# Kernel tuning notes

Hardware: AMD Instinct MI355X
Metric: run time of the kernel (lower is better)

The kernel has to match this reference:

```python
import jax, jax.numpy as jnp
import numpy as np

NUM_NODES = 100000
OUT_CHANNELS = 32
NUM_EDGES = 3200000


def setup_inputs() -> dict:
    key = jax.random.key(0)
    k1, k2, k3 = jax.random.split(key, 3)
    edge_index = jax.random.randint(k1, (2, NUM_EDGES), 0, NUM_NODES, dtype=jnp.int64)
    # nn.Linear init: weight [out, in], uniform(-1/sqrt(in), 1/sqrt(in))
    bound = 1.0 / np.sqrt(NUM_NODES)
    W = jax.random.uniform(k2, (OUT_CHANNELS, NUM_NODES), jnp.float32, -bound, bound)
    b = jax.random.uniform(k3, (OUT_CHANNELS,), jnp.float32, -bound, bound)
    return {"edge_index": edge_index, "W": W, "b": b}


def reference(edge_index, W, b):
    # LINK forward: A = sparse COO [N, num_nodes] with 1.0 per edge (duplicates sum),
    # logits = A @ W.T + b. Implemented as gather + segment_sum (no dense A).
    row = edge_index[0]
    col = edge_index[1]
    row = row - row.min()  # faithful to `row = row - row.min()`
    gathered = jnp.take(W.T, col, axis=0)  # [E, out_channels]
    logits = jax.ops.segment_sum(gathered, row, num_segments=NUM_NODES)  # [N, out]
    return logits + b
```

## Files before the change

kernel.cpp:

```cpp
#include <hip/hip_runtime.h>

#define NUM_NODES 100000
#define OUT_CH 32
#define NUM_EDGES 3200000

#define RPB 128
#define NB 782
#define NBG 783
#define CAP2 5120
#define FTPB 1024
#define TRB 782
#define BINB 250
#define TILE 12800
#define KPT 13
#define TPB 512

static __device__ __forceinline__ unsigned short f32_to_bf16_rne(float f) {
    unsigned u = __float_as_uint(f);
    unsigned r = u + 0x7FFFu + ((u >> 16) & 1u);
    return (unsigned short)(r >> 16);
}
static __device__ __forceinline__ float bf16_to_f32(unsigned short h) {
    return __uint_as_float(((unsigned)h) << 16);
}

__global__ void __launch_bounds__(FTPB)
fused_pre(const float* __restrict__ W, ushort4* __restrict__ Wt,
          const int* __restrict__ edge, int* __restrict__ partmin,
          int* __restrict__ bcount, unsigned int* __restrict__ bin) {
    int bk = blockIdx.x;
    int t  = threadIdx.x;
    if (bk < TRB) {
        __shared__ float tile[32][129];
        int tx = t & 127, ty = t >> 7;
        int colBase = bk * 128;
        int col = colBase + tx;
        if (col < NUM_NODES) {
            #pragma unroll
            for (int k = 0; k < 4; k++) {
                int c = ty + 8 * k;
                tile[c][tx] = W[(size_t)c * NUM_NODES + col];
            }
        }
        __syncthreads();
        int lc = t >> 3, q = t & 7;
        int ocol = colBase + lc;
        if (ocol < NUM_NODES) {
            ushort4 o;
            o.x = f32_to_bf16_rne(tile[q * 4 + 0][lc]);
            o.y = f32_to_bf16_rne(tile[q * 4 + 1][lc]);
            o.z = f32_to_bf16_rne(tile[q * 4 + 2][lc]);
            o.w = f32_to_bf16_rne(tile[q * 4 + 3][lc]);
            Wt[(size_t)ocol * 8 + q] = o;
        }
    } else {
        int mb = bk - TRB;
        __shared__ int cnt[NB];
        __shared__ int cur[NB];
        __shared__ int wm[16];
        for (int i = t; i < NB; i += FTPB) cnt[i] = 0;
        __syncthreads();
        int base = mb * TILE;
        unsigned int ent[KPT];
        int bb[KPT];
        int rm = 0x7fffffff;
        #pragma unroll
        for (int k = 0; k < KPT; k++) {
            int o = k * FTPB + t;
            bb[k] = -1;
            if (o < TILE) {
                int e = base + o;
                int r = edge[e];
                int c = edge[NUM_EDGES + e];
                rm = min(rm, r);
                int b = r >> 7;
                bb[k]  = b;
                ent[k] = ((unsigned int)(r & 127) << 17) | (unsigned int)c;
                atomicAdd(&cnt[b], 1);
            }
        }
        #pragma unroll
        for (int off = 32; off > 0; off >>= 1) rm = min(rm, __shfl_down(rm, off, 64));
        if ((t & 63) == 0) wm[t >> 6] = rm;
        __syncthreads();
        if (t == 0) {
            int m = wm[0];
            #pragma unroll
            for (int w = 1; w < 16; w++) m = min(m, wm[w]);
            partmin[mb] = m;
        }
        for (int i = t; i < NB; i += FTPB) cur[i] = cnt[i] ? atomicAdd(&bcount[i], cnt[i]) : 0;
        __syncthreads();
        #pragma unroll
        for (int k = 0; k < KPT; k++) {
            if (bb[k] >= 0) {
                int pos = atomicAdd(&cur[bb[k]], 1);
                if (pos < CAP2) bin[(size_t)bb[k] * CAP2 + pos] = ent[k];
            }
        }
    }
}

__global__ void __launch_bounds__(TPB)
bucket_gather(const unsigned int* __restrict__ bin, const int* __restrict__ bcount,
              const int* __restrict__ partmin,
              const ushort4* __restrict__ Wt, const float* __restrict__ b,
              float* __restrict__ out) {
    __shared__ int cnt2[RPB * 8];
    __shared__ int cur2[RPB * 8];
    __shared__ int rowstart[RPB];
    __shared__ int rowcnt[RPB];
    __shared__ int scn[RPB];
    __shared__ int lcol[CAP2];
    __shared__ int wmin[8];
    __shared__ int rminS;

    int t = threadIdx.x;
    int bk = blockIdx.x;
    int pm = (t < BINB) ? partmin[t] : 0x7fffffff;
    #pragma unroll
    for (int off = 32; off > 0; off >>= 1) pm = min(pm, __shfl_down(pm, off, 64));
    if ((t & 63) == 0) wmin[t >> 6] = pm;

    int n = (bk < NB) ? bcount[bk] : 0;
    if (n > CAP2) n = CAP2;
    const unsigned int* mybin = bin + (size_t)bk * CAP2;

    for (int i = t; i < RPB * 8; i += TPB) cnt2[i] = 0;
    __syncthreads();
    if (t == 0) {
        int m = wmin[0];
        #pragma unroll
        for (int w = 1; w < 8; w++) m = min(m, wmin[w]);
        rminS = m;
    }

    for (int i = t; i < n; i += TPB) {
        unsigned int p = mybin[i];
        int lr  = p >> 17;
        int seg = (p & 0x1FFFF) >> 14;
        atomicAdd(&cnt2[(lr << 3) | seg], 1);
    }
    __syncthreads();

    if (t < RPB) {
        int s = 0;
        #pragma unroll
        for (int k = 0; k < 8; k++) s += cnt2[(t << 3) | k];
        rowcnt[t] = s;
        scn[t] = s;
    }
    __syncthreads();
    for (int off = 1; off < RPB; off <<= 1) {
        int v = (t < RPB && t >= off) ? scn[t - off] : 0;
        __syncthreads();
        if (t < RPB) scn[t] += v;
        __syncthreads();
    }
    if (t < RPB) {
        int rs = scn[t] - rowcnt[t];
        rowstart[t] = rs;
        int run = rs;
        #pragma unroll
        for (int k = 0; k < 8; k++) { cur2[(t << 3) | k] = run; run += cnt2[(t << 3) | k]; }
    }
    __syncthreads();

    for (int i = t; i < n; i += TPB) {
        unsigned int p = mybin[i];
        int lr = p >> 17;
        int c  = p & 0x1FFFF;
        int pos = atomicAdd(&cur2[(lr << 3) | (c >> 14)], 1);
        lcol[pos] = c;
    }
    __syncthreads();

    int g   = t >> 3;
    int sub = t & 7;
    float4 bias = ((const float4*)b)[sub];
    int rmin = rminS;
    int lrA = g, lrB = g + 64;
    int outA = bk * RPB + lrA - rmin;
    int outB = bk * RPB + lrB - rmin;
    bool vA = (unsigned)outA < NUM_NODES;
    bool vB = (unsigned)outB < NUM_NODES;
    int iA = rowstart[lrA], eA = iA + rowcnt[lrA];
    int iB = rowstart[lrB], eB = iB + rowcnt[lrB];
    if (!vA) { iA = eA = 0; }
    if (!vB) { iB = eB = 0; }
    float4 accA = bias, accB = bias;
    int nPair = min(eA - iA, eB - iB);
    for (int k = 0; k < nPair; k++) {
        ushort4 wA = Wt[(size_t)lcol[iA + k] * 8 + sub];
        ushort4 wB = Wt[(size_t)lcol[iB + k] * 8 + sub];
        accA.x += bf16_to_f32(wA.x); accA.y += bf16_to_f32(wA.y);
        accA.z += bf16_to_f32(wA.z); accA.w += bf16_to_f32(wA.w);
        accB.x += bf16_to_f32(wB.x); accB.y += bf16_to_f32(wB.y);
        accB.z += bf16_to_f32(wB.z); accB.w += bf16_to_f32(wB.w);
    }
    iA += nPair; iB += nPair;
    for (; iA < eA; iA++) {
        ushort4 w = Wt[(size_t)lcol[iA] * 8 + sub];
        accA.x += bf16_to_f32(w.x); accA.y += bf16_to_f32(w.y);
        accA.z += bf16_to_f32(w.z); accA.w += bf16_to_f32(w.w);
    }
    for (; iB < eB; iB++) {
        ushort4 w = Wt[(size_t)lcol[iB] * 8 + sub];
        accB.x += bf16_to_f32(w.x); accB.y += bf16_to_f32(w.y);
        accB.z += bf16_to_f32(w.z); accB.w += bf16_to_f32(w.w);
    }
    if (vA) ((float4*)out)[(size_t)outA * 8 + sub] = accA;
    if (vB) ((float4*)out)[(size_t)outB * 8 + sub] = accB;
}

extern "C" void kernel_launch(void* const* d_in, const int* in_sizes, int n_in,
                              void* d_out, int out_size, void* d_ws, size_t ws_size,
                              hipStream_t stream) {
    const int*   edge = (const int*)d_in[0];
    const float* W    = (const float*)d_in[1];
    const float* b    = (const float*)d_in[2];
    float* out = (float*)d_out;

    char* ws = (char*)d_ws;
    int*          partmin = (int*)ws;
    int*          bcount  = (int*)(ws + 1024);
    ushort4*      Wt      = (ushort4*)(ws + 8192);
    unsigned int* bin     = (unsigned int*)(ws + 6422528);

    hipMemsetAsync(bcount, 0, NBG * sizeof(int), stream);
    fused_pre<<<TRB + BINB, FTPB, 0, stream>>>(W, Wt, edge, partmin, bcount, bin);
    bucket_gather<<<NBG, TPB, 0, stream>>>(bin, bcount, partmin, Wt, b, out);
}
```

Baseline: 151.9 us.

## Split each row bucket across two blocks and unroll the gather loop by four

The gather kernel now launches two 256-thread blocks per 128-row bucket. Each block filters the bucket's entries down to its own 64 rows, which shrinks shared memory and raises the block count to improve occupancy and latency hiding. The inner accumulation loop is unrolled by four, so eight independent Wt loads are in flight per iteration. The cost is that each bucket's bin is read twice. The per-half column buffer (CAPH) could overflow if a half-bucket holds more than 2560 entries.

```diff
diff --git a/kernel.cpp b/kernel.cpp
--- a/kernel.cpp
+++ b/kernel.cpp
@@ -13,7 +13,9 @@
 #define BINB 250
 #define TILE 12800
 #define KPT 13
-#define TPB 512
+#define GTPB 256
+#define CAPH 2560
+#define GGRID 1568
 
 static __device__ __forceinline__ unsigned short f32_to_bf16_rne(float f) {
     unsigned u = __float_as_uint(f);
@@ -89,7 +91,8 @@
             for (int w = 1; w < 16; w++) m = min(m, wm[w]);
             partmin[mb] = m;
         }
-        for (int i = t; i < NB; i += FTPB) cur[i] = cnt[i] ? atomicAdd(&bcount[i], cnt[i]) : 0;
+        for (int i = t; i < NB; i += FTPB)
+            cur[i] = cnt[i] ? atomicAdd(&bcount[i], cnt[i]) : 0;
         __syncthreads();
         #pragma unroll
         for (int k = 0; k < KPT; k++) {
@@ -101,49 +104,50 @@
     }
 }
 
-__global__ void __launch_bounds__(TPB)
+__global__ void __launch_bounds__(GTPB)
 bucket_gather(const unsigned int* __restrict__ bin, const int* __restrict__ bcount,
               const int* __restrict__ partmin,
               const ushort4* __restrict__ Wt, const float* __restrict__ b,
               float* __restrict__ out) {
-    __shared__ int cnt2[RPB * 8];
-    __shared__ int cur2[RPB * 8];
-    __shared__ int rowstart[RPB];
-    __shared__ int rowcnt[RPB];
-    __shared__ int scn[RPB];
-    __shared__ int lcol[CAP2];
-    __shared__ int wmin[8];
+    __shared__ int cnt2[64 * 8];
+    __shared__ int cur2[64 * 8];
+    __shared__ int rowstart[64];
+    __shared__ int rowcnt[64];
+    __shared__ int scn[64];
+    __shared__ int lcol[CAPH];
+    __shared__ int wmin[4];
     __shared__ int rminS;
 
-    int t = threadIdx.x;
+    int t  = threadIdx.x;
     int bk = blockIdx.x;
+    int gb   = ((bk >> 4) << 3) | (bk & 7);
+    int hbit = ((bk >> 3) & 1) << 6;
+
     int pm = (t < BINB) ? partmin[t] : 0x7fffffff;
     #pragma unroll
     for (int off = 32; off > 0; off >>= 1) pm = min(pm, __shfl_down(pm, off, 64));
     if ((t & 63) == 0) wmin[t >> 6] = pm;
 
-    int n = (bk < NB) ? bcount[bk] : 0;
+    int n = (gb < NB) ? bcount[gb] : 0;
     if (n > CAP2) n = CAP2;
-    const unsigned int* mybin = bin + (size_t)bk * CAP2;
-
-    for (int i = t; i < RPB * 8; i += TPB) cnt2[i] = 0;
-    __syncthreads();
-    if (t == 0) {
-        int m = wmin[0];
-        #pragma unroll
-        for (int w = 1; w < 8; w++) m = min(m, wmin[w]);
-        rminS = m;
-    }
-
-    for (int i = t; i < n; i += TPB) {
+    const unsigned int* mybin = bin + (size_t)gb * CAP2;
+
+    for (int i = t; i < 64 * 8; i += GTPB) cnt2[i] = 0;
+    __syncthreads();
+    if (t == 0)
+        rminS = min(min(wmin[0], wmin[1]), min(wmin[2], wmin[3]));
+
+    for (int i = t; i < n; i += GTPB) {
         unsigned int p = mybin[i];
-        int lr  = p >> 17;
-        int seg = (p & 0x1FFFF) >> 14;
-        atomicAdd(&cnt2[(lr << 3) | seg], 1);
-    }
-    __syncthreads();
-
-    if (t < RPB) {
+        int lr = p >> 17;
+        if ((lr & 64) == hbit) {
+            int seg = (p & 0x1FFFF) >> 14;
+            atomicAdd(&cnt2[((lr & 63) << 3) | seg], 1);
+        }
+    }
+    __syncthreads();
+
+    if (t < 64) {
         int s = 0;
         #pragma unroll
         for (int k = 0; k < 8; k++) s += cnt2[(t << 3) | k];
@@ -151,13 +155,13 @@
         scn[t] = s;
     }
     __syncthreads();
-    for (int off = 1; off < RPB; off <<= 1) {
-        int v = (t < RPB && t >= off) ? scn[t - off] : 0;
-        __syncthreads();
-        if (t < RPB) scn[t] += v;
-        __syncthreads();
-    }
-    if (t < RPB) {
+    for (int off = 1; off < 64; off <<= 1) {
+        int v = (t < 64 && t >= off) ? scn[t - off] : 0;
+        __syncthreads();
+        if (t < 64) scn[t] += v;
+        __syncthreads();
+    }
+    if (t < 64) {
         int rs = scn[t] - rowcnt[t];
         rowstart[t] = rs;
         int run = rs;
@@ -166,12 +170,14 @@
     }
     __syncthreads();
 
-    for (int i = t; i < n; i += TPB) {
+    for (int i = t; i < n; i += GTPB) {
         unsigned int p = mybin[i];
         int lr = p >> 17;
-        int c  = p & 0x1FFFF;
-        int pos = atomicAdd(&cur2[(lr << 3) | (c >> 14)], 1);
-        lcol[pos] = c;
+        if ((lr & 64) == hbit) {
+            int c = p & 0x1FFFF;
+            int pos = atomicAdd(&cur2[((lr & 63) << 3) | (c >> 14)], 1);
+            lcol[pos] = c;
+        }
     }
     __syncthreads();
 
@@ -179,18 +185,41 @@
     int sub = t & 7;
     float4 bias = ((const float4*)b)[sub];
     int rmin = rminS;
-    int lrA = g, lrB = g + 64;
-    int outA = bk * RPB + lrA - rmin;
-    int outB = bk * RPB + lrB - rmin;
+    int rowbase = gb * RPB + hbit;
+    int outA = rowbase + g - rmin;
+    int outB = rowbase + g + 32 - rmin;
     bool vA = (unsigned)outA < NUM_NODES;
     bool vB = (unsigned)outB < NUM_NODES;
-    int iA = rowstart[lrA], eA = iA + rowcnt[lrA];
-    int iB = rowstart[lrB], eB = iB + rowcnt[lrB];
+    int iA = rowstart[g],      eA = iA + rowcnt[g];
+    int iB = rowstart[g + 32], eB = iB + rowcnt[g + 32];
     if (!vA) { iA = eA = 0; }
     if (!vB) { iB = eB = 0; }
     float4 accA = bias, accB = bias;
     int nPair = min(eA - iA, eB - iB);
-    for (int k = 0; k < nPair; k++) {
+    int k = 0;
+    for (; k + 4 <= nPair; k += 4) {
+        int cA0 = lcol[iA + k],     cA1 = lcol[iA + k + 1];
+        int cA2 = lcol[iA + k + 2], cA3 = lcol[iA + k + 3];
+        int cB0 = lcol[iB + k],     cB1 = lcol[iB + k + 1];
+        int cB2 = lcol[iB + k + 2], cB3 = lcol[iB + k + 3];
+        ushort4 a0 = Wt[(size_t)cA0 * 8 + sub];
+        ushort4 a1 = Wt[(size_t)cA1 * 8 + sub];
+        ushort4 a2 = Wt[(size_t)cA2 * 8 + sub];
+        ushort4 a3 = Wt[(size_t)cA3 * 8 + sub];
+        ushort4 b0 = Wt[(size_t)cB0 * 8 + sub];
+        ushort4 b1 = Wt[(size_t)cB1 * 8 + sub];
+        ushort4 b2 = Wt[(size_t)cB2 * 8 + sub];
+        ushort4 b3 = Wt[(size_t)cB3 * 8 + sub];
+        accA.x += (bf16_to_f32(a0.x) + bf16_to_f32(a1.x)) + (bf16_to_f32(a2.x) + bf16_to_f32(a3.x));
+        accA.y += (bf16_to_f32(a0.y) + bf16_to_f32(a1.y)) + (bf16_to_f32(a2.y) + bf16_to_f32(a3.y));
+        accA.z += (bf16_to_f32(a0.z) + bf16_to_f32(a1.z)) + (bf16_to_f32(a2.z) + bf16_to_f32(a3.z));
+        accA.w += (bf16_to_f32(a0.w) + bf16_to_f32(a1.w)) + (bf16_to_f32(a2.w) + bf16_to_f32(a3.w));
+        accB.x += (bf16_to_f32(b0.x) + bf16_to_f32(b1.x)) + (bf16_to_f32(b2.x) + bf16_to_f32(b3.x));
+        accB.y += (bf16_to_f32(b0.y) + bf16_to_f32(b1.y)) + (bf16_to_f32(b2.y) + bf16_to_f32(b3.y));
+        accB.z += (bf16_to_f32(b0.z) + bf16_to_f32(b1.z)) + (bf16_to_f32(b2.z) + bf16_to_f32(b3.z));
+        accB.w += (bf16_to_f32(b0.w) + bf16_to_f32(b1.w)) + (bf16_to_f32(b2.w) + bf16_to_f32(b3.w));
+    }
+    for (; k < nPair; k++) {
         ushort4 wA = Wt[(size_t)lcol[iA + k] * 8 + sub];
         ushort4 wB = Wt[(size_t)lcol[iB + k] * 8 + sub];
         accA.x += bf16_to_f32(wA.x); accA.y += bf16_to_f32(wA.y);
@@ -229,5 +258,5 @@
 
     hipMemsetAsync(bcount, 0, NBG * sizeof(int), stream);
     fused_pre<<<TRB + BINB, FTPB, 0, stream>>>(W, Wt, edge, partmin, bcount, bin);
-    bucket_gather<<<NBG, TPB, 0, stream>>>(bin, bcount, partmin, Wt, b, out);
-}
+    bucket_gather<<<GGRID, GTPB, 0, stream>>>(bin, bcount, partmin, Wt, b, out);
+}
```

Measured after the change: 158.9 us. 4.6% more time.

## Split output channels into halves across blocks with half-major bf16 weight layout

Applied to the files above, without the earlier changes.

Stores the bf16 transposed weights as two channel halves, each a contiguous 16-channel slab, and launches twice as many 256-thread gather blocks, each handling one bucket for one half. Blocks for the same bucket half are grouped so each half's working set in cache is smaller. The per-row column-segment sub-sort is dropped in favour of a plain per-row counting sort, bin reads are vectorised and nontemporal, and the gather loop is unrolled by two. The cost is that each bucket's bin is read and counting-sorted twice, once per half.

```diff
diff --git a/kernel.cpp b/kernel.cpp
--- a/kernel.cpp
+++ b/kernel.cpp
@@ -6,14 +6,18 @@
 
 #define RPB 128
 #define NB 782
-#define NBG 783
+#define NBKT 784
 #define CAP2 5120
 #define FTPB 1024
 #define TRB 782
 #define BINB 250
 #define TILE 12800
 #define KPT 13
-#define TPB 512
+#define GTPB 256
+#define GGRID 1568
+
+typedef unsigned int uint4e  __attribute__((ext_vector_type(4)));
+typedef float        float4e __attribute__((ext_vector_type(4)));
 
 static __device__ __forceinline__ unsigned short f32_to_bf16_rne(float f) {
     unsigned u = __float_as_uint(f);
@@ -51,7 +55,7 @@
             o.y = f32_to_bf16_rne(tile[q * 4 + 1][lc]);
             o.z = f32_to_bf16_rne(tile[q * 4 + 2][lc]);
             o.w = f32_to_bf16_rne(tile[q * 4 + 3][lc]);
-            Wt[(size_t)ocol * 8 + q] = o;
+            Wt[(size_t)(q >> 2) * (NUM_NODES * 4) + (size_t)ocol * 4 + (q & 3)] = o;
         }
     } else {
         int mb = bk - TRB;
@@ -89,7 +93,8 @@
             for (int w = 1; w < 16; w++) m = min(m, wm[w]);
             partmin[mb] = m;
         }
-        for (int i = t; i < NB; i += FTPB) cur[i] = cnt[i] ? atomicAdd(&bcount[i], cnt[i]) : 0;
+        for (int i = t; i < NB; i += FTPB)
+            cur[i] = cnt[i] ? atomicAdd(&bcount[i], cnt[i]) : 0;
         __syncthreads();
         #pragma unroll
         for (int k = 0; k < KPT; k++) {
@@ -101,55 +106,54 @@
     }
 }
 
-__global__ void __launch_bounds__(TPB)
+__global__ void __launch_bounds__(GTPB)
 bucket_gather(const unsigned int* __restrict__ bin, const int* __restrict__ bcount,
               const int* __restrict__ partmin,
               const ushort4* __restrict__ Wt, const float* __restrict__ b,
               float* __restrict__ out) {
-    __shared__ int cnt2[RPB * 8];
-    __shared__ int cur2[RPB * 8];
+    __shared__ int cnt[RPB];
+    __shared__ int cur[RPB];
     __shared__ int rowstart[RPB];
-    __shared__ int rowcnt[RPB];
     __shared__ int scn[RPB];
     __shared__ int lcol[CAP2];
-    __shared__ int wmin[8];
+    __shared__ int wmin[4];
     __shared__ int rminS;
 
-    int t = threadIdx.x;
+    int t  = threadIdx.x;
     int bk = blockIdx.x;
+    int bkt  = ((bk >> 3) << 2) | (bk & 3);
+    int half = (bk >> 2) & 1;
+
     int pm = (t < BINB) ? partmin[t] : 0x7fffffff;
     #pragma unroll
     for (int off = 32; off > 0; off >>= 1) pm = min(pm, __shfl_down(pm, off, 64));
     if ((t & 63) == 0) wmin[t >> 6] = pm;
 
-    int n = (bk < NB) ? bcount[bk] : 0;
+    int n = (bkt < NB) ? bcount[bkt] : 0;
     if (n > CAP2) n = CAP2;
-    const unsigned int* mybin = bin + (size_t)bk * CAP2;
-
-    for (int i = t; i < RPB * 8; i += TPB) cnt2[i] = 0;
-    __syncthreads();
-    if (t == 0) {
-        int m = wmin[0];
-        #pragma unroll
-        for (int w = 1; w < 8; w++) m = min(m, wmin[w]);
-        rminS = m;
-    }
-
-    for (int i = t; i < n; i += TPB) {
-        unsigned int p = mybin[i];
-        int lr  = p >> 17;
-        int seg = (p & 0x1FFFF) >> 14;
-        atomicAdd(&cnt2[(lr << 3) | seg], 1);
-    }
-    __syncthreads();
-
-    if (t < RPB) {
-        int s = 0;
-        #pragma unroll
-        for (int k = 0; k < 8; k++) s += cnt2[(t << 3) | k];
-        rowcnt[t] = s;
-        scn[t] = s;
-    }
+    const unsigned int* mybin = bin + (size_t)bkt * CAP2;
+
+    if (t < RPB) cnt[t] = 0;
+    __syncthreads();
+    if (t == 0)
+        rminS = min(min(wmin[0], wmin[1]), min(wmin[2], wmin[3]));
+
+    int n4 = n >> 2;
+    const uint4e* mybin4 = (const uint4e*)mybin;
+    for (int i = t; i < n4; i += GTPB) {
+        uint4e p = __builtin_nontemporal_load(&mybin4[i]);
+        atomicAdd(&cnt[p.x >> 17], 1);
+        atomicAdd(&cnt[p.y >> 17], 1);
+        atomicAdd(&cnt[p.z >> 17], 1);
+        atomicAdd(&cnt[p.w >> 17], 1);
+    }
+    for (int i = (n4 << 2) + t; i < n; i += GTPB) {
+        unsigned int p = __builtin_nontemporal_load(&mybin[i]);
+        atomicAdd(&cnt[p >> 17], 1);
+    }
+    __syncthreads();
+
+    if (t < RPB) scn[t] = cnt[t];
     __syncthreads();
     for (int off = 1; off < RPB; off <<= 1) {
         int v = (t < RPB && t >= off) ? scn[t - off] : 0;
@@ -158,41 +162,62 @@
         __syncthreads();
     }
     if (t < RPB) {
-        int rs = scn[t] - rowcnt[t];
+        int rs = scn[t] - cnt[t];
         rowstart[t] = rs;
-        int run = rs;
-        #pragma unroll
-        for (int k = 0; k < 8; k++) { cur2[(t << 3) | k] = run; run += cnt2[(t << 3) | k]; }
-    }
-    __syncthreads();
-
-    for (int i = t; i < n; i += TPB) {
-        unsigned int p = mybin[i];
-        int lr = p >> 17;
-        int c  = p & 0x1FFFF;
-        int pos = atomicAdd(&cur2[(lr << 3) | (c >> 14)], 1);
-        lcol[pos] = c;
-    }
-    __syncthreads();
-
-    int g   = t >> 3;
-    int sub = t & 7;
-    float4 bias = ((const float4*)b)[sub];
+        cur[t] = rs;
+    }
+    __syncthreads();
+
+    for (int i = t; i < n4; i += GTPB) {
+        uint4e p = __builtin_nontemporal_load(&mybin4[i]);
+        int p0 = atomicAdd(&cur[p.x >> 17], 1); lcol[p0] = p.x & 0x1FFFF;
+        int p1 = atomicAdd(&cur[p.y >> 17], 1); lcol[p1] = p.y & 0x1FFFF;
+        int p2 = atomicAdd(&cur[p.z >> 17], 1); lcol[p2] = p.z & 0x1FFFF;
+        int p3 = atomicAdd(&cur[p.w >> 17], 1); lcol[p3] = p.w & 0x1FFFF;
+    }
+    for (int i = (n4 << 2) + t; i < n; i += GTPB) {
+        unsigned int p = __builtin_nontemporal_load(&mybin[i]);
+        int pos = atomicAdd(&cur[p >> 17], 1);
+        lcol[pos] = p & 0x1FFFF;
+    }
+    __syncthreads();
+
+    int g   = t >> 2;
+    int sub = t & 3;
+    const ushort4* Wth = Wt + (size_t)half * (NUM_NODES * 4);
+    float4 bias = ((const float4*)b)[half * 4 + sub];
     int rmin = rminS;
     int lrA = g, lrB = g + 64;
-    int outA = bk * RPB + lrA - rmin;
-    int outB = bk * RPB + lrB - rmin;
+    int outA = bkt * RPB + lrA - rmin;
+    int outB = bkt * RPB + lrB - rmin;
     bool vA = (unsigned)outA < NUM_NODES;
     bool vB = (unsigned)outB < NUM_NODES;
-    int iA = rowstart[lrA], eA = iA + rowcnt[lrA];
-    int iB = rowstart[lrB], eB = iB + rowcnt[lrB];
+    int iA = rowstart[lrA], eA = iA + cnt[lrA];
+    int iB = rowstart[lrB], eB = iB + cnt[lrB];
     if (!vA) { iA = eA = 0; }
     if (!vB) { iB = eB = 0; }
     float4 accA = bias, accB = bias;
     int nPair = min(eA - iA, eB - iB);
-    for (int k = 0; k < nPair; k++) {
-        ushort4 wA = Wt[(size_t)lcol[iA + k] * 8 + sub];
-        ushort4 wB = Wt[(size_t)lcol[iB + k] * 8 + sub];
+    int k = 0;
+    for (; k + 2 <= nPair; k += 2) {
+        int cA0 = lcol[iA + k], cA1 = lcol[iA + k + 1];
+        int cB0 = lcol[iB + k], cB1 = lcol[iB + k + 1];
+        ushort4 a0 = Wth[(size_t)cA0 * 4 + sub];
+        ushort4 a1 = Wth[(size_t)cA1 * 4 + sub];
+        ushort4 b0 = Wth[(size_t)cB0 * 4 + sub];
+        ushort4 b1 = Wth[(size_t)cB1 * 4 + sub];
+        accA.x += bf16_to_f32(a0.x) + bf16_to_f32(a1.x);
+        accA.y += bf16_to_f32(a0.y) + bf16_to_f32(a1.y);
+        accA.z += bf16_to_f32(a0.z) + bf16_to_f32(a1.z);
+        accA.w += bf16_to_f32(a0.w) + bf16_to_f32(a1.w);
+        accB.x += bf16_to_f32(b0.x) + bf16_to_f32(b1.x);
+        accB.y += bf16_to_f32(b0.y) + bf16_to_f32(b1.y);
+        accB.z += bf16_to_f32(b0.z) + bf16_to_f32(b1.z);
+        accB.w += bf16_to_f32(b0.w) + bf16_to_f32(b1.w);
+    }
+    for (; k < nPair; k++) {
+        ushort4 wA = Wth[(size_t)lcol[iA + k] * 4 + sub];
+        ushort4 wB = Wth[(size_t)lcol[iB + k] * 4 + sub];
         accA.x += bf16_to_f32(wA.x); accA.y += bf16_to_f32(wA.y);
         accA.z += bf16_to_f32(wA.z); accA.w += bf16_to_f32(wA.w);
         accB.x += bf16_to_f32(wB.x); accB.y += bf16_to_f32(wB.y);
@@ -200,17 +225,19 @@
     }
     iA += nPair; iB += nPair;
     for (; iA < eA; iA++) {
-        ushort4 w = Wt[(size_t)lcol[iA] * 8 + sub];
+        ushort4 w = Wth[(size_t)lcol[iA] * 4 + sub];
         accA.x += bf16_to_f32(w.x); accA.y += bf16_to_f32(w.y);
         accA.z += bf16_to_f32(w.z); accA.w += bf16_to_f32(w.w);
     }
     for (; iB < eB; iB++) {
-        ushort4 w = Wt[(size_t)lcol[iB] * 8 + sub];
+        ushort4 w = Wth[(size_t)lcol[iB] * 4 + sub];
         accB.x += bf16_to_f32(w.x); accB.y += bf16_to_f32(w.y);
         accB.z += bf16_to_f32(w.z); accB.w += bf16_to_f32(w.w);
     }
-    if (vA) ((float4*)out)[(size_t)outA * 8 + sub] = accA;
-    if (vB) ((float4*)out)[(size_t)outB * 8 + sub] = accB;
+    float4e oA = { accA.x, accA.y, accA.z, accA.w };
+    float4e oB = { accB.x, accB.y, accB.z, accB.w };
+    if (vA) __builtin_nontemporal_store(oA, &((float4e*)out)[(size_t)outA * 8 + half * 4 + sub]);
+    if (vB) __builtin_nontemporal_store(oB, &((float4e*)out)[(size_t)outB * 8 + half * 4 + sub]);
 }
 
 extern "C" void kernel_launch(void* const* d_in, const int* in_sizes, int n_in,
@@ -227,7 +254,7 @@
     ushort4*      Wt      = (ushort4*)(ws + 8192);
     unsigned int* bin     = (unsigned int*)(ws + 6422528);
 
-    hipMemsetAsync(bcount, 0, NBG * sizeof(int), stream);
+    hipMemsetAsync(bcount, 0, NBKT * sizeof(int), stream);
     fused_pre<<<TRB + BINB, FTPB, 0, stream>>>(W, Wt, edge, partmin, bcount, bin);
-    bucket_gather<<<NBG, TPB, 0, stream>>>(bin, bcount, partmin, Wt, b, out);
-}
+    bucket_gather<<<GGRID, GTPB, 0, stream>>>(bin, bcount, partmin, Wt, b, out);
+}
```

Measured after the change: 154.6 us. Within noise of the previous version (+1.8%).
